# Performance work log

Measured on AMD Instinct MI355X. Metric: run time of the kernel, lower is better.

Reference implementation:

```python
import jax, jax.numpy as jnp
import numpy as np

ALPHA = 1.0
EPS = 1e-9
MASK_FILL = 100000.0  # large value pushes masked entries to the end of ascending sort


def setup_inputs() -> dict:
    key = jax.random.key(0)
    k1, k2, k3, k4 = jax.random.split(key, 4)
    bs, nh, n = 128, 32, 2048
    input1 = jax.random.normal(k1, (bs, 4, nh, n), dtype=jnp.float32)
    input2 = jax.random.normal(k2, (bs, 1, nh, n), dtype=jnp.float32)
    mask1 = jax.random.randint(k3, (bs, 4, nh, n), 0, 2).astype(jnp.int32)
    mask2 = jax.random.randint(k4, (bs, 1, nh, n), 0, 2).astype(jnp.int32)
    return {"input1": input1, "mask1": mask1, "input2": input2, "mask2": mask2}


def reference(input1, mask1, input2, mask2):
    # input1: (bs, 4, nh, n) scores; input2/mask2: (bs, 1, nh, n) targets/mask.
    # mask1 is unused by the original forward.
    i2 = jnp.where(mask2 > 0, input2, jnp.float32(MASK_FILL))
    idx = jnp.argsort(i2, axis=-1)                                  # (bs, 1, nh, n)
    mask_sorted = jnp.take_along_axis(mask2, idx, axis=-1).astype(jnp.float32)
    idx4 = jnp.broadcast_to(idx, input1.shape)                      # repeat over the 4 choices
    inputs_sorted = jnp.take_along_axis(input1, idx4, axis=-1)      # (bs, 4, nh, n)
    proj = jnp.exp(ALPHA * inputs_sorted) * mask_sorted             # mode='exp'
    proj_cum = jnp.cumsum(proj, axis=-1) * mask_sorted
    prob = jnp.prod((proj + EPS) / (proj_cum + EPS), axis=-1)       # (bs, 4, nh)
    return jnp.transpose(prob, (0, 2, 1))                           # (bs, nh, 4)
```

## Files before the change

### kernel.cpp

```cpp
#include <hip/hip_runtime.h>

#define N   2048
#define NT  128
#define EPK 16

typedef unsigned int u32;

__device__ __forceinline__ u32 fkey(float f) {
  u32 u = __float_as_uint(f);
  return (u & 0x80000000u) ? ~u : (u | 0x80000000u);
}

__device__ __forceinline__ u32 umin32(u32 a, u32 b) { return a < b ? a : b; }
__device__ __forceinline__ u32 umax32(u32 a, u32 b) { return a < b ? b : a; }

template <int CTRL, int RM, int BM, bool BC>
__device__ __forceinline__ float dppf(float v) {
  int r = __builtin_amdgcn_update_dpp(0, __float_as_int(v), CTRL, RM, BM, BC);
  return __int_as_float(r);
}

template <int D>
__device__ __forceinline__ u32 exch(u32 x, int lane) {
  if constexpr (D == 1) {
    return (u32)__builtin_amdgcn_update_dpp((int)x, (int)x, 0xB1, 0xF, 0xF, true);
  } else if constexpr (D == 2) {
    return (u32)__builtin_amdgcn_update_dpp((int)x, (int)x, 0x4E, 0xF, 0xF, true);
  } else if constexpr (D == 4) {
    return (u32)__builtin_amdgcn_ds_swizzle((int)x, 0x101F);
  } else if constexpr (D == 8) {
    return (u32)__builtin_amdgcn_update_dpp((int)x, (int)x, 0x128, 0xF, 0xF, true);
  } else if constexpr (D == 16) {
    int a = (int)x, b = (int)x;
    asm("v_permlane16_swap_b32 %0, %1" : "+v"(a), "+v"(b));
    return (lane & 16) ? (u32)a : (u32)b;
  } else {
    int a = (int)x, b = (int)x;
    asm("v_permlane32_swap_b32 %0, %1" : "+v"(a), "+v"(b));
    return (lane & 32) ? (u32)a : (u32)b;
  }
}

template <int D>
__device__ __forceinline__ void sh_pass(u32* kv, bool keep_min, int lane) {
#pragma unroll
  for (int m = 0; m < EPK; ++m) {
    u32 o = exch<D>(kv[m], lane);
    u32 mn = umin32(kv[m], o), mx = umax32(kv[m], o);
    kv[m] = keep_min ? mn : mx;
  }
}

#define INPASS(J, UPEXPR)                               \
  {                                                     \
    _Pragma("unroll")                                   \
    for (int m = 0; m < EPK; ++m)                       \
      if ((m & (J)) == 0) {                             \
        const bool up_ = (UPEXPR);                      \
        u32 x = kv[m], y = kv[m | (J)];                 \
        u32 mn = umin32(x, y), mx = umax32(x, y);       \
        kv[m] = up_ ? mn : mx;                          \
        kv[m | (J)] = up_ ? mx : mn;                    \
      }                                                 \
  }

__device__ __forceinline__ float wave_scan_incl(float x) {
  x += dppf<0x111, 0xF, 0xF, true>(x);
  x += dppf<0x112, 0xF, 0xF, true>(x);
  x += dppf<0x114, 0xF, 0xF, true>(x);
  x += dppf<0x118, 0xF, 0xF, true>(x);
  x += dppf<0x142, 0xA, 0xF, false>(x);
  x += dppf<0x143, 0xC, 0xF, false>(x);
  return x;
}

__device__ __forceinline__ float wave_prod64(float x, int lane) {
  x *= dppf<0xB1, 0xF, 0xF, true>(x);
  x *= dppf<0x4E, 0xF, 0xF, true>(x);
  x *= dppf<0x141, 0xF, 0xF, true>(x);
  x *= dppf<0x140, 0xF, 0xF, true>(x);
  {
    int a = __float_as_int(x), b = __float_as_int(x);
    asm("v_permlane16_swap_b32 %0, %1" : "+v"(a), "+v"(b));
    x *= __int_as_float((lane & 16) ? a : b);
  }
  {
    int a = __float_as_int(x), b = __float_as_int(x);
    asm("v_permlane32_swap_b32 %0, %1" : "+v"(a), "+v"(b));
    x *= __int_as_float((lane & 32) ? a : b);
  }
  return x;
}

__device__ __forceinline__ void stage_row_full(const float* __restrict__ r1,
                                               float* buf, int lane) {
#pragma unroll
  for (int q = 0; q < 8; ++q) {
    const float4* src = (const float4*)r1 + (q * 64 + lane);
    char* dst = (char*)buf + q * 1024;
    __builtin_amdgcn_global_load_lds(
        (const __attribute__((address_space(1))) unsigned int*)src,
        (__attribute__((address_space(3))) unsigned int*)dst, 16, 0, 0);
  }
}

__global__ __launch_bounds__(NT) void listmle_kernel(
    const float* __restrict__ input1,
    const float* __restrict__ input2,
    const int* __restrict__ mask2,
    float* __restrict__ out) {
  __shared__ __align__(16) u32 slab[N];
  __shared__ __align__(16) float rowbuf[N];

  const int tid = threadIdx.x;
  const int lane = tid & 63;
  const int w = tid >> 6;
  const int p = blockIdx.x;
  const int b = p >> 5, h = p & 31;

  {
    const float4* i2v = (const float4*)(input2 + (size_t)p * N);
    const int4* m2v = (const int4*)(mask2 + (size_t)p * N);
#pragma unroll
    for (int q = 0; q < 4; ++q) {
      float4 vv = i2v[tid + 128 * q];
      int4 mm = m2v[tid + 128 * q];
      const u32 i0 = 4u * (u32)(tid + 128 * q);
      float vs[4] = {vv.x, vv.y, vv.z, vv.w};
      int ms[4] = {mm.x, mm.y, mm.z, mm.w};
#pragma unroll
      for (int r = 0; r < 4; ++r) {
        u32 idx = i0 + r;
        u32 key = (ms[r] > 0) ? ((fkey(vs[r]) & 0xFFFFF800u) | idx)
                              : (0xFFFFF800u | idx);
        slab[idx ^ ((idx >> 5) & 31u)] = key;
      }
    }
  }

  if (w == 0)
    stage_row_full(input1 + ((size_t)((b * 4 + 0) * 32 + h)) * N, rowbuf, lane);

  __syncthreads();
  u32 kv[EPK];
#pragma unroll
  for (int m = 0; m < EPK; ++m) {
    u32 idx = (u32)(w * 1024 + lane * EPK + m);
    kv[m] = slab[idx ^ ((idx >> 5) & 31u)];
  }

  INPASS(1, (m & 2) == 0)
  INPASS(2, (m & 4) == 0) INPASS(1, (m & 4) == 0)
  INPASS(4, (m & 8) == 0) INPASS(2, (m & 8) == 0) INPASS(1, (m & 8) == 0)
  {
    const bool up = (lane & 1) == 0;
    INPASS(8, up) INPASS(4, up) INPASS(2, up) INPASS(1, up)
  }
  {
    const bool up = (lane & 2) == 0;
    sh_pass<1>(kv, ((lane & 1) == 0) == up, lane);
    INPASS(8, up) INPASS(4, up) INPASS(2, up) INPASS(1, up)
  }
  {
    const bool up = (lane & 4) == 0;
    sh_pass<2>(kv, ((lane & 2) == 0) == up, lane);
    sh_pass<1>(kv, ((lane & 1) == 0) == up, lane);
    INPASS(8, up) INPASS(4, up) INPASS(2, up) INPASS(1, up)
  }
  {
    const bool up = (lane & 8) == 0;
    sh_pass<4>(kv, ((lane & 4) == 0) == up, lane);
    sh_pass<2>(kv, ((lane & 2) == 0) == up, lane);
    sh_pass<1>(kv, ((lane & 1) == 0) == up, lane);
    INPASS(8, up) INPASS(4, up) INPASS(2, up) INPASS(1, up)
  }
  {
    const bool up = (lane & 16) == 0;
    sh_pass<8>(kv, ((lane & 8) == 0) == up, lane);
    sh_pass<4>(kv, ((lane & 4) == 0) == up, lane);
    sh_pass<2>(kv, ((lane & 2) == 0) == up, lane);
    sh_pass<1>(kv, ((lane & 1) == 0) == up, lane);
    INPASS(8, up) INPASS(4, up) INPASS(2, up) INPASS(1, up)
  }
  {
    const bool up = (lane & 32) == 0;
    sh_pass<16>(kv, ((lane & 16) == 0) == up, lane);
    sh_pass<8>(kv, ((lane & 8) == 0) == up, lane);
    sh_pass<4>(kv, ((lane & 4) == 0) == up, lane);
    sh_pass<2>(kv, ((lane & 2) == 0) == up, lane);
    sh_pass<1>(kv, ((lane & 1) == 0) == up, lane);
    INPASS(8, up) INPASS(4, up) INPASS(2, up) INPASS(1, up)
  }
  {
    const bool up = (w == 0);
    sh_pass<32>(kv, ((lane & 32) == 0) == up, lane);
    sh_pass<16>(kv, ((lane & 16) == 0) == up, lane);
    sh_pass<8>(kv, ((lane & 8) == 0) == up, lane);
    sh_pass<4>(kv, ((lane & 4) == 0) == up, lane);
    sh_pass<2>(kv, ((lane & 2) == 0) == up, lane);
    sh_pass<1>(kv, ((lane & 1) == 0) == up, lane);
    INPASS(8, up) INPASS(4, up) INPASS(2, up) INPASS(1, up)
  }
  {
    __syncthreads();
#pragma unroll
    for (int m = 0; m < EPK; ++m) slab[w * 1024 + m * 64 + lane] = kv[m];
    __syncthreads();
#pragma unroll
    for (int m = 0; m < EPK; ++m) {
      u32 o = slab[(w ^ 1) * 1024 + m * 64 + lane];
      kv[m] = (w == 0) ? umin32(kv[m], o) : umax32(kv[m], o);
    }
    __syncthreads();
    sh_pass<32>(kv, (lane & 32) == 0, lane);
    sh_pass<16>(kv, (lane & 16) == 0, lane);
    sh_pass<8>(kv, (lane & 8) == 0, lane);
    sh_pass<4>(kv, (lane & 4) == 0, lane);
    sh_pass<2>(kv, (lane & 2) == 0, lane);
    sh_pass<1>(kv, (lane & 1) == 0, lane);
    INPASS(8, true) INPASS(4, true) INPASS(2, true) INPASS(1, true)
  }

  {
    u32* pairs = slab;
#pragma unroll
    for (int t = 0; t < EPK / 2; ++t) {
      u32 a = kv[2 * t], b2 = kv[2 * t + 1];
      u32 ia = (a & 0x7FFu) | ((a < 0xFFFFF800u) ? 0x800u : 0u);
      u32 ib = (b2 & 0x7FFu) | ((b2 < 0xFFFFF800u) ? 0x800u : 0u);
      u32 slot = (u32)(w * 512 + lane * 8 + t);
      pairs[slot ^ ((slot >> 5) & 31u)] = ia | (ib << 16);
    }
  }
  __syncthreads();
  u32 pk[EPK];
#pragma unroll
  for (int t = 0; t < EPK; ++t) {
    u32 slot = (u32)(lane * 16 + t);
    pk[t] = slab[slot ^ ((slot >> 5) & 31u)];
  }
  __syncthreads();

  if (w == 1)
    stage_row_full(input1 + ((size_t)((b * 4 + 2) * 32 + h)) * N, (float*)slab, lane);

  float* mybuf = (w == 0) ? rowbuf : (float*)slab;
#pragma unroll
  for (int cc = 0; cc < 2; ++cc) {
    const int c = 2 * w + cc;
    asm volatile("s_waitcnt vmcnt(0)" ::: "memory");

    float e[32];
    float lsum = 0.f;
#pragma unroll
    for (int m = 0; m < 32; ++m) {
      u32 info = (pk[m >> 1] >> ((m & 1) * 16)) & 0xFFFFu;
      float v = mybuf[info & 0x7FFu];
      float pe = (info & 0x800u) ? __expf(v) : 0.f;
      e[m] = pe;
      lsum += pe;
    }

    if (cc == 0) {
      asm volatile("s_waitcnt lgkmcnt(0)" ::: "memory");
      stage_row_full(input1 + ((size_t)((b * 4 + c + 1) * 32 + h)) * N, mybuf, lane);
    }

    float inc = wave_scan_incl(lsum);
    float cum = inc - lsum;

    float prod = 1.f;
#pragma unroll
    for (int m = 0; m < 32; ++m) {
      cum += e[m];
      u32 info = pk[m >> 1] >> ((m & 1) * 16);
      if (info & 0x800u) prod *= __fdividef(e[m] + 1e-9f, cum + 1e-9f);
    }
    prod = wave_prod64(prod, lane);
    if (lane == 0) out[(size_t)p * 4 + c] = prod;
  }
}

extern "C" void kernel_launch(void* const* d_in, const int* in_sizes, int n_in,
                              void* d_out, int out_size, void* d_ws, size_t ws_size,
                              hipStream_t stream) {
  const float* input1 = (const float*)d_in[0];
  const float* input2 = (const float*)d_in[2];
  const int* mask2 = (const int*)d_in[3];
  float* out = (float*)d_out;

  const int problems = 128 * 32;
  listmle_kernel<<<problems, NT, 0, stream>>>(input1, input2, mask2, out);
}
```

Before: 77.27 us.

## Use four waves per block with one input1 row per wave

Doubles the block to 256 threads so each wave sorts 512 keys (8 per lane) and then handles one of the four score rows. The bitonic sort gains cross-wave exchange stages through LDS with lightweight barriers. All four input1 rows are prefetched into LDS at kernel start instead of being double-buffered. This is meant to raise parallelism and shorten the serial sort and scan path per block, at the cost of more LDS per block (40KB) and extra cross-wave exchange rounds.

```diff
diff --git a/kernel.cpp b/kernel.cpp
--- a/kernel.cpp
+++ b/kernel.cpp
@@ -1,8 +1,8 @@
 #include <hip/hip_runtime.h>
 
 #define N   2048
-#define NT  128
-#define EPK 16
+#define NT  256
+#define EPK 8
 
 typedef unsigned int u32;
 
@@ -19,6 +19,13 @@
   int r = __builtin_amdgcn_update_dpp(0, __float_as_int(v), CTRL, RM, BM, BC);
   return __int_as_float(r);
 }
+
+#define RAWBAR()                                          \
+  do {                                                    \
+    asm volatile("s_waitcnt lgkmcnt(0)" ::: "memory");    \
+    __builtin_amdgcn_s_barrier();                         \
+    asm volatile("" ::: "memory");                        \
+  } while (0)
 
 template <int D>
 __device__ __forceinline__ u32 exch(u32 x, int lane) {
@@ -64,6 +71,21 @@
       }                                                 \
   }
 
+#define XW(PW, KEEPMIN)                                                     \
+  {                                                                         \
+    RAWBAR();                                                               \
+    _Pragma("unroll")                                                       \
+    for (int m = 0; m < EPK; ++m) slab[w * 512 + m * 64 + lane] = kv[m];    \
+    RAWBAR();                                                               \
+    const bool km_ = (KEEPMIN);                                             \
+    _Pragma("unroll")                                                       \
+    for (int m = 0; m < EPK; ++m) {                                         \
+      u32 o = slab[(PW) * 512 + m * 64 + lane];                             \
+      u32 mn = umin32(kv[m], o), mx = umax32(kv[m], o);                     \
+      kv[m] = km_ ? mn : mx;                                                \
+    }                                                                       \
+  }
+
 __device__ __forceinline__ float wave_scan_incl(float x) {
   x += dppf<0x111, 0xF, 0xF, true>(x);
   x += dppf<0x112, 0xF, 0xF, true>(x);
@@ -104,13 +126,13 @@
   }
 }
 
-__global__ __launch_bounds__(NT) void listmle_kernel(
+__global__ __launch_bounds__(NT, 4) void listmle_kernel(
     const float* __restrict__ input1,
     const float* __restrict__ input2,
     const int* __restrict__ mask2,
     float* __restrict__ out) {
+  __shared__ __align__(16) float rows[4][N];
   __shared__ __align__(16) u32 slab[N];
-  __shared__ __align__(16) float rowbuf[N];
 
   const int tid = threadIdx.x;
   const int lane = tid & 63;
@@ -118,14 +140,16 @@
   const int p = blockIdx.x;
   const int b = p >> 5, h = p & 31;
 
+  stage_row_full(input1 + ((size_t)((b * 4 + w) * 32 + h)) * N, rows[w], lane);
+
   {
     const float4* i2v = (const float4*)(input2 + (size_t)p * N);
     const int4* m2v = (const int4*)(mask2 + (size_t)p * N);
 #pragma unroll
-    for (int q = 0; q < 4; ++q) {
-      float4 vv = i2v[tid + 128 * q];
-      int4 mm = m2v[tid + 128 * q];
-      const u32 i0 = 4u * (u32)(tid + 128 * q);
+    for (int q = 0; q < 2; ++q) {
+      float4 vv = i2v[tid + 256 * q];
+      int4 mm = m2v[tid + 256 * q];
+      const u32 i0 = 4u * (u32)(tid + 256 * q);
       float vs[4] = {vv.x, vv.y, vv.z, vv.w};
       int ms[4] = {mm.x, mm.y, mm.z, mm.w};
 #pragma unroll
@@ -137,42 +161,37 @@
       }
     }
   }
-
-  if (w == 0)
-    stage_row_full(input1 + ((size_t)((b * 4 + 0) * 32 + h)) * N, rowbuf, lane);
-
-  __syncthreads();
+  RAWBAR();
   u32 kv[EPK];
 #pragma unroll
   for (int m = 0; m < EPK; ++m) {
-    u32 idx = (u32)(w * 1024 + lane * EPK + m);
+    u32 idx = (u32)(w * 512 + lane * EPK + m);
     kv[m] = slab[idx ^ ((idx >> 5) & 31u)];
   }
 
   INPASS(1, (m & 2) == 0)
   INPASS(2, (m & 4) == 0) INPASS(1, (m & 4) == 0)
-  INPASS(4, (m & 8) == 0) INPASS(2, (m & 8) == 0) INPASS(1, (m & 8) == 0)
   {
     const bool up = (lane & 1) == 0;
-    INPASS(8, up) INPASS(4, up) INPASS(2, up) INPASS(1, up)
+    INPASS(4, up) INPASS(2, up) INPASS(1, up)
   }
   {
     const bool up = (lane & 2) == 0;
     sh_pass<1>(kv, ((lane & 1) == 0) == up, lane);
-    INPASS(8, up) INPASS(4, up) INPASS(2, up) INPASS(1, up)
+    INPASS(4, up) INPASS(2, up) INPASS(1, up)
   }
   {
     const bool up = (lane & 4) == 0;
     sh_pass<2>(kv, ((lane & 2) == 0) == up, lane);
     sh_pass<1>(kv, ((lane & 1) == 0) == up, lane);
-    INPASS(8, up) INPASS(4, up) INPASS(2, up) INPASS(1, up)
+    INPASS(4, up) INPASS(2, up) INPASS(1, up)
   }
   {
     const bool up = (lane & 8) == 0;
     sh_pass<4>(kv, ((lane & 4) == 0) == up, lane);
     sh_pass<2>(kv, ((lane & 2) == 0) == up, lane);
     sh_pass<1>(kv, ((lane & 1) == 0) == up, lane);
-    INPASS(8, up) INPASS(4, up) INPASS(2, up) INPASS(1, up)
+    INPASS(4, up) INPASS(2, up) INPASS(1, up)
   }
   {
     const bool up = (lane & 16) == 0;
@@ -180,7 +199,7 @@
     sh_pass<4>(kv, ((lane & 4) == 0) == up, lane);
     sh_pass<2>(kv, ((lane & 2) == 0) == up, lane);
     sh_pass<1>(kv, ((lane & 1) == 0) == up, lane);
-    INPASS(8, up) INPASS(4, up) INPASS(2, up) INPASS(1, up)
+    INPASS(4, up) INPASS(2, up) INPASS(1, up)
   }
   {
     const bool up = (lane & 32) == 0;
@@ -189,96 +208,81 @@
     sh_pass<4>(kv, ((lane & 4) == 0) == up, lane);
     sh_pass<2>(kv, ((lane & 2) == 0) == up, lane);
     sh_pass<1>(kv, ((lane & 1) == 0) == up, lane);
-    INPASS(8, up) INPASS(4, up) INPASS(2, up) INPASS(1, up)
-  }
-  {
-    const bool up = (w == 0);
+    INPASS(4, up) INPASS(2, up) INPASS(1, up)
+  }
+  {
+    const bool up = (w & 1) == 0;
     sh_pass<32>(kv, ((lane & 32) == 0) == up, lane);
     sh_pass<16>(kv, ((lane & 16) == 0) == up, lane);
     sh_pass<8>(kv, ((lane & 8) == 0) == up, lane);
     sh_pass<4>(kv, ((lane & 4) == 0) == up, lane);
     sh_pass<2>(kv, ((lane & 2) == 0) == up, lane);
     sh_pass<1>(kv, ((lane & 1) == 0) == up, lane);
-    INPASS(8, up) INPASS(4, up) INPASS(2, up) INPASS(1, up)
-  }
-  {
-    __syncthreads();
-#pragma unroll
-    for (int m = 0; m < EPK; ++m) slab[w * 1024 + m * 64 + lane] = kv[m];
-    __syncthreads();
-#pragma unroll
-    for (int m = 0; m < EPK; ++m) {
-      u32 o = slab[(w ^ 1) * 1024 + m * 64 + lane];
-      kv[m] = (w == 0) ? umin32(kv[m], o) : umax32(kv[m], o);
-    }
-    __syncthreads();
+    INPASS(4, up) INPASS(2, up) INPASS(1, up)
+  }
+  {
+    const bool up = (w & 2) == 0;
+    XW(w ^ 1, ((w & 1) == 0) == up);
+    sh_pass<32>(kv, ((lane & 32) == 0) == up, lane);
+    sh_pass<16>(kv, ((lane & 16) == 0) == up, lane);
+    sh_pass<8>(kv, ((lane & 8) == 0) == up, lane);
+    sh_pass<4>(kv, ((lane & 4) == 0) == up, lane);
+    sh_pass<2>(kv, ((lane & 2) == 0) == up, lane);
+    sh_pass<1>(kv, ((lane & 1) == 0) == up, lane);
+    INPASS(4, up) INPASS(2, up) INPASS(1, up)
+  }
+  {
+    XW(w ^ 2, (w & 2) == 0);
+    XW(w ^ 1, (w & 1) == 0);
     sh_pass<32>(kv, (lane & 32) == 0, lane);
     sh_pass<16>(kv, (lane & 16) == 0, lane);
     sh_pass<8>(kv, (lane & 8) == 0, lane);
     sh_pass<4>(kv, (lane & 4) == 0, lane);
     sh_pass<2>(kv, (lane & 2) == 0, lane);
     sh_pass<1>(kv, (lane & 1) == 0, lane);
-    INPASS(8, true) INPASS(4, true) INPASS(2, true) INPASS(1, true)
-  }
-
-  {
-    u32* pairs = slab;
-#pragma unroll
-    for (int t = 0; t < EPK / 2; ++t) {
-      u32 a = kv[2 * t], b2 = kv[2 * t + 1];
-      u32 ia = (a & 0x7FFu) | ((a < 0xFFFFF800u) ? 0x800u : 0u);
-      u32 ib = (b2 & 0x7FFu) | ((b2 < 0xFFFFF800u) ? 0x800u : 0u);
-      u32 slot = (u32)(w * 512 + lane * 8 + t);
-      pairs[slot ^ ((slot >> 5) & 31u)] = ia | (ib << 16);
-    }
-  }
-  __syncthreads();
-  u32 pk[EPK];
-#pragma unroll
-  for (int t = 0; t < EPK; ++t) {
-    u32 slot = (u32)(lane * 16 + t);
-    pk[t] = slab[slot ^ ((slot >> 5) & 31u)];
-  }
-  __syncthreads();
-
-  if (w == 1)
-    stage_row_full(input1 + ((size_t)((b * 4 + 2) * 32 + h)) * N, (float*)slab, lane);
-
-  float* mybuf = (w == 0) ? rowbuf : (float*)slab;
-#pragma unroll
-  for (int cc = 0; cc < 2; ++cc) {
-    const int c = 2 * w + cc;
-    asm volatile("s_waitcnt vmcnt(0)" ::: "memory");
-
-    float e[32];
-    float lsum = 0.f;
-#pragma unroll
-    for (int m = 0; m < 32; ++m) {
-      u32 info = (pk[m >> 1] >> ((m & 1) * 16)) & 0xFFFFu;
-      float v = mybuf[info & 0x7FFu];
-      float pe = (info & 0x800u) ? __expf(v) : 0.f;
-      e[m] = pe;
-      lsum += pe;
-    }
-
-    if (cc == 0) {
-      asm volatile("s_waitcnt lgkmcnt(0)" ::: "memory");
-      stage_row_full(input1 + ((size_t)((b * 4 + c + 1) * 32 + h)) * N, mybuf, lane);
-    }
-
-    float inc = wave_scan_incl(lsum);
-    float cum = inc - lsum;
-
-    float prod = 1.f;
-#pragma unroll
-    for (int m = 0; m < 32; ++m) {
-      cum += e[m];
-      u32 info = pk[m >> 1] >> ((m & 1) * 16);
-      if (info & 0x800u) prod *= __fdividef(e[m] + 1e-9f, cum + 1e-9f);
-    }
-    prod = wave_prod64(prod, lane);
-    if (lane == 0) out[(size_t)p * 4 + c] = prod;
-  }
+    INPASS(4, true) INPASS(2, true) INPASS(1, true)
+  }
+
+  RAWBAR();
+#pragma unroll
+  for (int t = 0; t < EPK / 2; ++t) {
+    u32 a = kv[2 * t], b2 = kv[2 * t + 1];
+    u32 ia = (a & 0x7FFu) | ((a < 0xFFFFF800u) ? 0x800u : 0u);
+    u32 ib = (b2 & 0x7FFu) | ((b2 < 0xFFFFF800u) ? 0x800u : 0u);
+    u32 P = (u32)(w * 256 + lane * 4 + t);
+    slab[(P & 15u) * 64 + (P >> 4)] = ia | (ib << 16);
+  }
+  RAWBAR();
+  u32 pk[16];
+#pragma unroll
+  for (int t = 0; t < 16; ++t) pk[t] = slab[t * 64 + lane];
+
+  const float* mybuf = rows[w];
+  asm volatile("s_waitcnt vmcnt(0)" ::: "memory");
+
+  float e[32];
+  float lsum = 0.f;
+#pragma unroll
+  for (int m = 0; m < 32; ++m) {
+    u32 info = (pk[m >> 1] >> ((m & 1) * 16)) & 0xFFFFu;
+    float v = mybuf[info & 0x7FFu];
+    float pe = (info & 0x800u) ? __expf(v) : 0.f;
+    e[m] = pe;
+    lsum += pe;
+  }
+
+  float inc = wave_scan_incl(lsum);
+  float cum = inc - lsum;
+
+  float prod = 1.f;
+#pragma unroll
+  for (int m = 0; m < 32; ++m) {
+    cum += e[m];
+    u32 info = pk[m >> 1] >> ((m & 1) * 16);
+    if (info & 0x800u) prod *= __fdividef(e[m] + 1e-9f, cum + 1e-9f);
+  }
+  prod = wave_prod64(prod, lane);
+  if (lane == 0) out[(size_t)p * 4 + w] = prod;
 }
 
 extern "C" void kernel_launch(void* const* d_in, const int* in_sizes, int n_in,
```

Result: no change. 77.64 us (+0.5%).
